# Kernel optimization log

Hardware: AMD Instinct MI355X
Metric: run time of the kernel (lower is better)

## Reference

```python
import jax, jax.numpy as jnp
import numpy as np

FEATURE = 1024
HIDDEN = 1024
BS = 64
T = 512


def setup_inputs() -> dict:
    key = jax.random.key(0)
    ks = jax.random.split(key, 5)
    # xavier_normal with gain=0.1: std = 0.1*sqrt(2/(fan_in+fan_out))
    std = 0.1 * np.sqrt(2.0 / (HIDDEN + FEATURE + HIDDEN))
    return {
        "x": jax.random.normal(ks[0], (BS, T, FEATURE), dtype=jnp.float32),
        "h_0": jax.random.normal(ks[1], (BS, HIDDEN), dtype=jnp.float32),
        "w_z": std * jax.random.normal(ks[2], (HIDDEN + FEATURE, HIDDEN), dtype=jnp.float32),
        "w_r": std * jax.random.normal(ks[3], (HIDDEN + FEATURE, HIDDEN), dtype=jnp.float32),
        "w": std * jax.random.normal(ks[4], (HIDDEN + FEATURE, HIDDEN), dtype=jnp.float32),
        "biasZ": jnp.zeros((HIDDEN,), dtype=jnp.float32),
        "biasR": jnp.zeros((HIDDEN,), dtype=jnp.float32),
        "biasHbar": jnp.zeros((HIDDEN,), dtype=jnp.float32),
    }


def reference(x, h_0, w_z, w_r, w, biasZ, biasR, biasHbar):
    # Split weights into h-part and x-part so the x contributions for z/r can be
    # precomputed for ALL timesteps in one big GEMM (same math as concat+matmul).
    H = h_0.shape[1]
    wz_h, wz_x = w_z[:H], w_z[H:]
    wr_h, wr_x = w_r[:H], w_r[H:]
    w_h, w_x = w[:H], w[H:]

    # (bs, T, hidden) precomputed x-side gate pre-activations
    xz = jnp.einsum('btf,fh->bth', x, wz_x) + biasZ
    xr = jnp.einsum('btf,fh->bth', x, wr_x) + biasR
    xh = jnp.einsum('btf,fh->bth', x, w_x) + biasHbar

    def step(h, inp):
        xz_t, xr_t, xh_t = inp
        z_t = jax.nn.sigmoid(h @ wz_h + xz_t)
        r_t = jax.nn.sigmoid(h @ wr_h + xr_t)
        hbar_t = jnp.tanh((r_t * h) @ w_h + xh_t)
        h_new = (1.0 - z_t) * h + z_t * hbar_t
        return h_new, h_new

    # scan over time (leading axis), inputs transposed to (T, bs, hidden)
    xs = (xz.swapaxes(0, 1), xr.swapaxes(0, 1), xh.swapaxes(0, 1))
    h_n, out_t = jax.lax.scan(step, h_0, xs)
    output = out_t.swapaxes(0, 1)  # (bs, T, hidden)
    return output, h_n
```

## Files before the change

### kernel.cpp

```cpp
#include <hip/hip_runtime.h>
#include <hip/hip_bf16.h>
#include <stdint.h>

#define BS 64
#define TT 512
#define FEAT 1024
#define HID 1024

__device__ __forceinline__ float sigmoidf_(float x){ return 1.0f/(1.0f + __expf(-x)); }

__device__ __forceinline__ unsigned short f2bf(float f){
    __hip_bfloat16 h = __float2bfloat16(f);
    return *reinterpret_cast<unsigned short*>(&h);
}
__device__ __forceinline__ float bf2f(unsigned short u){
    __hip_bfloat16 h = *reinterpret_cast<__hip_bfloat16*>(&u);
    return __bfloat162float(h);
}

__global__ __launch_bounds__(256) void p1_gemm(
    const float* __restrict__ x,
    const float* __restrict__ w_z, const float* __restrict__ w_r, const float* __restrict__ w,
    const float* __restrict__ bZ, const float* __restrict__ bR, const float* __restrict__ bH,
    float* __restrict__ xz32, float* __restrict__ xr32,
    unsigned short* __restrict__ xz16, unsigned short* __restrict__ xr16,
    float* __restrict__ xh, int use_bf)
{
    __shared__ float As[32][136];
    __shared__ float Bs[32][72];

    const int m0   = blockIdx.x * 128;
    const int n0g  = blockIdx.y * 64;
    const int mat  = n0g >> 10;
    const int ncol = n0g & 1023;

    const float* Wm    = (mat==0) ? w_z : (mat==1) ? w_r : w;
    const float* Bbase = Wm + (size_t)HID*1024 + ncol;
    const float* bias  = ((mat==0) ? bZ : (mat==1) ? bR : bH) + ncol;

    const int tid = threadIdx.x;
    const int tx = tid & 15, ty = tid >> 4;
    const int lm = tid >> 3;
    const int lk = (tid & 7) * 4;

    float acc[8][4];
    #pragma unroll
    for (int i=0;i<8;i++)
        #pragma unroll
        for (int j=0;j<4;j++) acc[i][j] = 0.f;

    for (int k0 = 0; k0 < 1024; k0 += 32) {
        #pragma unroll
        for (int h = 0; h < 4; ++h) {
            const int m = lm + 32*h;
            float4 a = *(const float4*)(x + (size_t)(m0+m)*1024 + k0 + lk);
            const float av[4] = {a.x, a.y, a.z, a.w};
            #pragma unroll
            for (int i=0;i<4;i++) {
                const int kk  = lk + i;
                const int col = m ^ (((kk>>2)&3) << 3);
                As[kk][col] = av[i];
            }
        }
        {
            const int kk = tid >> 3;
            const int nq = (tid & 7) * 4;
            float4 b0 = *(const float4*)(Bbase + (size_t)(k0+kk)*1024 + nq);
            float4 b1 = *(const float4*)(Bbase + (size_t)(k0+kk)*1024 + nq + 32);
            *(float4*)&Bs[kk][nq]      = b0;
            *(float4*)&Bs[kk][nq + 32] = b1;
        }
        __syncthreads();
        #pragma unroll
        for (int kk = 0; kk < 32; ++kk) {
            const int ablk = (ty ^ ((kk>>2)&3)) << 3;
            float4 a0 = *(const float4*)&As[kk][ablk];
            float4 a1 = *(const float4*)&As[kk][ablk + 4];
            float4 b4 = *(const float4*)&Bs[kk][tx*4];
            const float av[8] = {a0.x,a0.y,a0.z,a0.w,a1.x,a1.y,a1.z,a1.w};
            const float bv[4] = {b4.x,b4.y,b4.z,b4.w};
            #pragma unroll
            for (int i=0;i<8;i++)
                #pragma unroll
                for (int j=0;j<4;j++)
                    acc[i][j] = fmaf(av[i], bv[j], acc[i][j]);
        }
        __syncthreads();
    }

    float4 bb = *(const float4*)(bias + tx*4);
    const float badd[4] = {bb.x, bb.y, bb.z, bb.w};
    #pragma unroll
    for (int i=0;i<8;i++) {
        const int m = m0 + ty*8 + i;
        const size_t off = (size_t)m*1024 + ncol + tx*4;
        float v[4];
        #pragma unroll
        for (int j=0;j<4;j++) v[j] = acc[i][j] + badd[j];
        if (mat == 2) {
            float4 o; o.x=v[0]; o.y=v[1]; o.z=v[2]; o.w=v[3];
            *(float4*)(xh + off) = o;
        } else if (!use_bf) {
            float* dst = (mat==0) ? xz32 : xr32;
            float4 o; o.x=v[0]; o.y=v[1]; o.z=v[2]; o.w=v[3];
            *(float4*)(dst + off) = o;
        } else {
            unsigned short* dst = (mat==0) ? xz16 : xr16;
            ushort4 u; u.x=f2bf(v[0]); u.y=f2bf(v[1]); u.z=f2bf(v[2]); u.w=f2bf(v[3]);
            *(ushort4*)(dst + off) = u;
        }
    }
}

__global__ __launch_bounds__(256) void tr_h0(const float* __restrict__ h0, float* __restrict__ hT)
{
    const int g = blockIdx.x*256 + threadIdx.x;
    const int b = g >> 10, j = g & 1023;
    hT[j*64 + b] = h0[g];
}

__global__ __launch_bounds__(256) void k_gates(
    const float* __restrict__ hT,
    const float* __restrict__ w_z, const float* __restrict__ w_r,
    const float* __restrict__ xz32, const float* __restrict__ xr32,
    const unsigned short* __restrict__ xz16, const unsigned short* __restrict__ xr16,
    float* __restrict__ zT, float* __restrict__ rhT, int t, int use_bf)
{
    __shared__ float part[4][8][64];
    const int wg   = blockIdx.x;
    const int lane = threadIdx.x & 63;
    const int wv   = __builtin_amdgcn_readfirstlane(threadIdx.x >> 6);
    const bool isR = (wg >= 128);
    const float* W = isR ? w_r : w_z;
    const int ccol = (wg & 127) * 8;

    const float* wp = W  + (size_t)(wv*256)*1024 + ccol;
    const float* hp = hT + (size_t)(wv*256)*64   + lane;

    float acc[8] = {0,0,0,0,0,0,0,0};
    #pragma unroll 8
    for (int k = 0; k < 256; ++k) {
        const float hk = hp[(size_t)k*64];
        float4 wa = *(const float4*)(wp + (size_t)k*1024);
        float4 wb = *(const float4*)(wp + (size_t)k*1024 + 4);
        acc[0] = fmaf(hk, wa.x, acc[0]); acc[1] = fmaf(hk, wa.y, acc[1]);
        acc[2] = fmaf(hk, wa.z, acc[2]); acc[3] = fmaf(hk, wa.w, acc[3]);
        acc[4] = fmaf(hk, wb.x, acc[4]); acc[5] = fmaf(hk, wb.y, acc[5]);
        acc[6] = fmaf(hk, wb.z, acc[6]); acc[7] = fmaf(hk, wb.w, acc[7]);
    }
    #pragma unroll
    for (int c=0;c<8;c++) part[wv][c][lane] = acc[c];
    __syncthreads();

    #pragma unroll
    for (int e=0;e<2;e++) {
        const int o = threadIdx.x + e*256;
        const int c = o >> 6, b = o & 63;
        const float s = part[0][c][b] + part[1][c][b] + part[2][c][b] + part[3][c][b];
        const int j = ccol + c;
        const size_t xoff = ((size_t)b*TT + t)*1024 + j;
        if (!isR) {
            const float xv = use_bf ? bf2f(xz16[xoff]) : xz32[xoff];
            zT[j*64 + b] = sigmoidf_(s + xv);
        } else {
            const float xv = use_bf ? bf2f(xr16[xoff]) : xr32[xoff];
            rhT[j*64 + b] = sigmoidf_(s + xv) * hT[j*64 + b];
        }
    }
}

__global__ __launch_bounds__(256) void k_hbar(
    float* __restrict__ hT, const float* __restrict__ rhT, const float* __restrict__ zT,
    const float* __restrict__ w, float* __restrict__ out, int t, int is_last)
{
    __shared__ float part[4][4][64];
    const int wg   = blockIdx.x;
    const int lane = threadIdx.x & 63;
    const int wv   = __builtin_amdgcn_readfirstlane(threadIdx.x >> 6);
    const int c0   = wg * 4;

    const float* wp = w   + (size_t)(wv*256)*1024 + c0;
    const float* rp = rhT + (size_t)(wv*256)*64   + lane;

    float acc[4] = {0,0,0,0};
    #pragma unroll 8
    for (int k = 0; k < 256; ++k) {
        const float rk = rp[(size_t)k*64];
        float4 wa = *(const float4*)(wp + (size_t)k*1024);
        acc[0] = fmaf(rk, wa.x, acc[0]); acc[1] = fmaf(rk, wa.y, acc[1]);
        acc[2] = fmaf(rk, wa.z, acc[2]); acc[3] = fmaf(rk, wa.w, acc[3]);
    }
    #pragma unroll
    for (int c=0;c<4;c++) part[wv][c][lane] = acc[c];
    __syncthreads();

    const int o = threadIdx.x;
    const int c = o >> 6, b = o & 63;
    const float s = part[0][c][b] + part[1][c][b] + part[2][c][b] + part[3][c][b];
    const int j = c0 + c;
    const size_t ooff = ((size_t)b*TT + t)*1024 + j;
    const float hb   = tanhf(s + out[ooff]);
    const float z    = zT[j*64 + b];
    const float hold = hT[j*64 + b];
    const float hn   = (1.f - z)*hold + z*hb;
    hT[j*64 + b] = hn;
    out[ooff]    = hn;
    if (is_last) out[(size_t)BS*TT*1024 + (size_t)b*1024 + j] = hn;
}

extern "C" void kernel_launch(void* const* d_in, const int* in_sizes, int n_in,
                              void* d_out, int out_size, void* d_ws, size_t ws_size,
                              hipStream_t stream)
{
    const float* x   = (const float*)d_in[0];
    const float* h0  = (const float*)d_in[1];
    const float* w_z = (const float*)d_in[2];
    const float* w_r = (const float*)d_in[3];
    const float* w   = (const float*)d_in[4];
    const float* bZ  = (const float*)d_in[5];
    const float* bR  = (const float*)d_in[6];
    const float* bH  = (const float*)d_in[7];
    float* out = (float*)d_out;

    const size_t nBT = (size_t)BS*TT*1024;
    const size_t need32 = (2*nBT + 3*65536) * 4;
    const int use_bf = (ws_size < need32) ? 1 : 0;

    char* wsb = (char*)d_ws;
    float *xz32 = nullptr, *xr32 = nullptr;
    unsigned short *xz16 = nullptr, *xr16 = nullptr;
    float *hT, *zT, *rhT;
    if (!use_bf) {
        xz32 = (float*)wsb;
        xr32 = xz32 + nBT;
        hT   = xr32 + nBT;
    } else {
        xz16 = (unsigned short*)wsb;
        xr16 = xz16 + nBT;
        hT   = (float*)(wsb + 2*nBT*sizeof(unsigned short));
    }
    zT  = hT + 65536;
    rhT = zT + 65536;

    p1_gemm<<<dim3(256,48), 256, 0, stream>>>(x, w_z, w_r, w, bZ, bR, bH,
                                              xz32, xr32, xz16, xr16, out, use_bf);
    tr_h0<<<256, 256, 0, stream>>>(h0, hT);
    for (int t = 0; t < TT; ++t) {
        k_gates<<<256, 256, 0, stream>>>(hT, w_z, w_r, xz32, xr32, xz16, xr16, zT, rhT, t, use_bf);
        k_hbar <<<256, 256, 0, stream>>>(hT, rhT, zT, w, out, t, (t == TT-1) ? 1 : 0);
    }
}
```

Measured before the change: 26.87 ms.

## Replace per-timestep kernel launches with persistent cooperative scan kernel

```diff
diff --git a/kernel.cpp b/kernel.cpp
--- a/kernel.cpp
+++ b/kernel.cpp
@@ -1,11 +1,16 @@
 #include <hip/hip_runtime.h>
 #include <hip/hip_bf16.h>
+#include <hip/hip_cooperative_groups.h>
 #include <stdint.h>
 
 #define BS 64
 #define TT 512
 #define FEAT 1024
 #define HID 1024
+#define NWG 256
+#define NTHR 512
+
+namespace cg = cooperative_groups;
 
 __device__ __forceinline__ float sigmoidf_(float x){ return 1.0f/(1.0f + __expf(-x)); }
 
@@ -22,9 +27,8 @@
     const float* __restrict__ x,
     const float* __restrict__ w_z, const float* __restrict__ w_r, const float* __restrict__ w,
     const float* __restrict__ bZ, const float* __restrict__ bR, const float* __restrict__ bH,
-    float* __restrict__ xz32, float* __restrict__ xr32,
     unsigned short* __restrict__ xz16, unsigned short* __restrict__ xr16,
-    float* __restrict__ xh, int use_bf)
+    float* __restrict__ xh)
 {
     __shared__ float As[32][136];
     __shared__ float Bs[32][72];
@@ -100,10 +104,6 @@
         if (mat == 2) {
             float4 o; o.x=v[0]; o.y=v[1]; o.z=v[2]; o.w=v[3];
             *(float4*)(xh + off) = o;
-        } else if (!use_bf) {
-            float* dst = (mat==0) ? xz32 : xr32;
-            float4 o; o.x=v[0]; o.y=v[1]; o.z=v[2]; o.w=v[3];
-            *(float4*)(dst + off) = o;
         } else {
             unsigned short* dst = (mat==0) ? xz16 : xr16;
             ushort4 u; u.x=f2bf(v[0]); u.y=f2bf(v[1]); u.z=f2bf(v[2]); u.w=f2bf(v[3]);
@@ -112,100 +112,114 @@
     }
 }
 
-__global__ __launch_bounds__(256) void tr_h0(const float* __restrict__ h0, float* __restrict__ hT)
+__global__ __launch_bounds__(NTHR, 1) void scan_persist(
+    const float* __restrict__ h0,
+    const float* __restrict__ w_z, const float* __restrict__ w_r, const float* __restrict__ w,
+    const unsigned short* __restrict__ xz16, const unsigned short* __restrict__ xr16,
+    float* __restrict__ hT, float* __restrict__ rhT, float* __restrict__ out)
 {
-    const int g = blockIdx.x*256 + threadIdx.x;
-    const int b = g >> 10, j = g & 1023;
-    hT[j*64 + b] = h0[g];
-}
-
-__global__ __launch_bounds__(256) void k_gates(
-    const float* __restrict__ hT,
-    const float* __restrict__ w_z, const float* __restrict__ w_r,
-    const float* __restrict__ xz32, const float* __restrict__ xr32,
-    const unsigned short* __restrict__ xz16, const unsigned short* __restrict__ xr16,
-    float* __restrict__ zT, float* __restrict__ rhT, int t, int use_bf)
-{
-    __shared__ float part[4][8][64];
-    const int wg   = blockIdx.x;
-    const int lane = threadIdx.x & 63;
-    const int wv   = __builtin_amdgcn_readfirstlane(threadIdx.x >> 6);
-    const bool isR = (wg >= 128);
-    const float* W = isR ? w_r : w_z;
-    const int ccol = (wg & 127) * 8;
-
-    const float* wp = W  + (size_t)(wv*256)*1024 + ccol;
-    const float* hp = hT + (size_t)(wv*256)*64   + lane;
-
-    float acc[8] = {0,0,0,0,0,0,0,0};
-    #pragma unroll 8
-    for (int k = 0; k < 256; ++k) {
-        const float hk = hp[(size_t)k*64];
-        float4 wa = *(const float4*)(wp + (size_t)k*1024);
-        float4 wb = *(const float4*)(wp + (size_t)k*1024 + 4);
-        acc[0] = fmaf(hk, wa.x, acc[0]); acc[1] = fmaf(hk, wa.y, acc[1]);
-        acc[2] = fmaf(hk, wa.z, acc[2]); acc[3] = fmaf(hk, wa.w, acc[3]);
-        acc[4] = fmaf(hk, wb.x, acc[4]); acc[5] = fmaf(hk, wb.y, acc[5]);
-        acc[6] = fmaf(hk, wb.z, acc[6]); acc[7] = fmaf(hk, wb.w, acc[7]);
-    }
-    #pragma unroll
-    for (int c=0;c<8;c++) part[wv][c][lane] = acc[c];
-    __syncthreads();
-
-    #pragma unroll
-    for (int e=0;e<2;e++) {
-        const int o = threadIdx.x + e*256;
-        const int c = o >> 6, b = o & 63;
-        const float s = part[0][c][b] + part[1][c][b] + part[2][c][b] + part[3][c][b];
-        const int j = ccol + c;
-        const size_t xoff = ((size_t)b*TT + t)*1024 + j;
-        if (!isR) {
-            const float xv = use_bf ? bf2f(xz16[xoff]) : xz32[xoff];
-            zT[j*64 + b] = sigmoidf_(s + xv);
-        } else {
-            const float xv = use_bf ? bf2f(xr16[xoff]) : xr32[xoff];
-            rhT[j*64 + b] = sigmoidf_(s + xv) * hT[j*64 + b];
-        }
-    }
-}
-
-__global__ __launch_bounds__(256) void k_hbar(
-    float* __restrict__ hT, const float* __restrict__ rhT, const float* __restrict__ zT,
-    const float* __restrict__ w, float* __restrict__ out, int t, int is_last)
-{
-    __shared__ float part[4][4][64];
-    const int wg   = blockIdx.x;
-    const int lane = threadIdx.x & 63;
-    const int wv   = __builtin_amdgcn_readfirstlane(threadIdx.x >> 6);
-    const int c0   = wg * 4;
-
-    const float* wp = w   + (size_t)(wv*256)*1024 + c0;
-    const float* rp = rhT + (size_t)(wv*256)*64   + lane;
-
-    float acc[4] = {0,0,0,0};
-    #pragma unroll 8
-    for (int k = 0; k < 256; ++k) {
-        const float rk = rp[(size_t)k*64];
-        float4 wa = *(const float4*)(wp + (size_t)k*1024);
-        acc[0] = fmaf(rk, wa.x, acc[0]); acc[1] = fmaf(rk, wa.y, acc[1]);
-        acc[2] = fmaf(rk, wa.z, acc[2]); acc[3] = fmaf(rk, wa.w, acc[3]);
-    }
-    #pragma unroll
-    for (int c=0;c<4;c++) part[wv][c][lane] = acc[c];
-    __syncthreads();
-
-    const int o = threadIdx.x;
-    const int c = o >> 6, b = o & 63;
-    const float s = part[0][c][b] + part[1][c][b] + part[2][c][b] + part[3][c][b];
-    const int j = c0 + c;
-    const size_t ooff = ((size_t)b*TT + t)*1024 + j;
-    const float hb   = tanhf(s + out[ooff]);
-    const float z    = zT[j*64 + b];
-    const float hold = hT[j*64 + b];
-    const float hn   = (1.f - z)*hold + z*hb;
-    hT[j*64 + b] = hn;
-    out[ooff]    = hn;
-    if (is_last) out[(size_t)BS*TT*1024 + (size_t)b*1024 + j] = hn;
+    cg::grid_group grid = cg::this_grid();
+
+    __shared__ float lwz[1024*4];
+    __shared__ float lwr[1024*4];
+    __shared__ float lwh[1024*4];
+    __shared__ float part[8*8*64];
+    __shared__ float zs[4*64];
+
+    const int wg  = blockIdx.x;
+    const int tid = threadIdx.x;
+    const int c0  = wg * 4;
+    const int q   = tid >> 6;
+    const int b   = tid & 63;
+
+    for (int k = tid; k < 1024; k += NTHR) {
+        *(float4*)&lwz[k*4] = *(const float4*)(w_z + (size_t)k*1024 + c0);
+        *(float4*)&lwr[k*4] = *(const float4*)(w_r + (size_t)k*1024 + c0);
+        *(float4*)&lwh[k*4] = *(const float4*)(w   + (size_t)k*1024 + c0);
+    }
+    {
+        const int g0 = wg * NTHR + tid;
+        if (g0 < HID*BS) {
+            const int bb = g0 >> 10, jj = g0 & 1023;
+            hT[jj*64 + bb] = h0[g0];
+        }
+    }
+    grid.sync();
+
+    for (int t = 0; t < TT; ++t) {
+        {
+            float az0=0.f,az1=0.f,az2=0.f,az3=0.f;
+            float ar0=0.f,ar1=0.f,ar2=0.f,ar3=0.f;
+            const float*  hp  = hT + (size_t)(q*128)*64 + b;
+            const float4* wzp = (const float4*)&lwz[(q*128)*4];
+            const float4* wrp = (const float4*)&lwr[(q*128)*4];
+            #pragma unroll 8
+            for (int kk = 0; kk < 128; ++kk) {
+                const float hk = hp[(size_t)kk*64];
+                const float4 wz4 = wzp[kk];
+                const float4 wr4 = wrp[kk];
+                az0 = fmaf(hk, wz4.x, az0); az1 = fmaf(hk, wz4.y, az1);
+                az2 = fmaf(hk, wz4.z, az2); az3 = fmaf(hk, wz4.w, az3);
+                ar0 = fmaf(hk, wr4.x, ar0); ar1 = fmaf(hk, wr4.y, ar1);
+                ar2 = fmaf(hk, wr4.z, ar2); ar3 = fmaf(hk, wr4.w, ar3);
+            }
+            part[(q*8+0)*64+b] = az0; part[(q*8+1)*64+b] = az1;
+            part[(q*8+2)*64+b] = az2; part[(q*8+3)*64+b] = az3;
+            part[(q*8+4)*64+b] = ar0; part[(q*8+5)*64+b] = ar1;
+            part[(q*8+6)*64+b] = ar2; part[(q*8+7)*64+b] = ar3;
+        }
+        __syncthreads();
+        {
+            const int a  = tid >> 6;
+            const int bb = tid & 63;
+            float s = 0.f;
+            #pragma unroll
+            for (int qq = 0; qq < 8; ++qq) s += part[(qq*8+a)*64+bb];
+            if (a < 4) {
+                const size_t xoff = ((size_t)bb*TT + t)*1024 + c0 + a;
+                zs[a*64+bb] = sigmoidf_(s + bf2f(xz16[xoff]));
+            } else {
+                const int c = a - 4;
+                const size_t xoff = ((size_t)bb*TT + t)*1024 + c0 + c;
+                const float rv = sigmoidf_(s + bf2f(xr16[xoff]));
+                rhT[(c0+c)*64 + bb] = rv * hT[(c0+c)*64 + bb];
+            }
+        }
+        grid.sync();
+
+        {
+            float ah0=0.f,ah1=0.f,ah2=0.f,ah3=0.f;
+            const float*  rp  = rhT + (size_t)(q*128)*64 + b;
+            const float4* whp = (const float4*)&lwh[(q*128)*4];
+            #pragma unroll 8
+            for (int kk = 0; kk < 128; ++kk) {
+                const float rk = rp[(size_t)kk*64];
+                const float4 w4 = whp[kk];
+                ah0 = fmaf(rk, w4.x, ah0); ah1 = fmaf(rk, w4.y, ah1);
+                ah2 = fmaf(rk, w4.z, ah2); ah3 = fmaf(rk, w4.w, ah3);
+            }
+            part[(q*4+0)*64+b] = ah0; part[(q*4+1)*64+b] = ah1;
+            part[(q*4+2)*64+b] = ah2; part[(q*4+3)*64+b] = ah3;
+        }
+        __syncthreads();
+        if (tid < 256) {
+            const int c  = tid >> 6;
+            const int bb = tid & 63;
+            float s = 0.f;
+            #pragma unroll
+            for (int qq = 0; qq < 8; ++qq) s += part[(qq*4+c)*64+bb];
+            const size_t ooff = ((size_t)bb*TT + t)*1024 + c0 + c;
+            const float hbar = tanhf(s + out[ooff]);
+            const float zv   = zs[c*64+bb];
+            const int   hoff = (c0+c)*64 + bb;
+            const float hold = hT[hoff];
+            const float hn   = fmaf(zv, hbar - hold, hold);
+            hT[hoff]  = hn;
+            out[ooff] = hn;
+            if (t == TT-1) out[(size_t)BS*TT*1024 + (size_t)bb*1024 + c0 + c] = hn;
+        }
+        grid.sync();
+    }
 }
 
 extern "C" void kernel_launch(void* const* d_in, const int* in_sizes, int n_in,
@@ -223,30 +237,20 @@
     float* out = (float*)d_out;
 
     const size_t nBT = (size_t)BS*TT*1024;
-    const size_t need32 = (2*nBT + 3*65536) * 4;
-    const int use_bf = (ws_size < need32) ? 1 : 0;
-
     char* wsb = (char*)d_ws;
-    float *xz32 = nullptr, *xr32 = nullptr;
-    unsigned short *xz16 = nullptr, *xr16 = nullptr;
-    float *hT, *zT, *rhT;
-    if (!use_bf) {
-        xz32 = (float*)wsb;
-        xr32 = xz32 + nBT;
-        hT   = xr32 + nBT;
-    } else {
-        xz16 = (unsigned short*)wsb;
-        xr16 = xz16 + nBT;
-        hT   = (float*)(wsb + 2*nBT*sizeof(unsigned short));
-    }
-    zT  = hT + 65536;
-    rhT = zT + 65536;
+    unsigned short* xz16 = (unsigned short*)wsb;
+    unsigned short* xr16 = xz16 + nBT;
+    float* hT  = (float*)(wsb + 2*nBT*sizeof(unsigned short));
+    float* rhT = hT + HID*BS;
 
     p1_gemm<<<dim3(256,48), 256, 0, stream>>>(x, w_z, w_r, w, bZ, bR, bH,
-                                              xz32, xr32, xz16, xr16, out, use_bf);
-    tr_h0<<<256, 256, 0, stream>>>(h0, hT);
-    for (int t = 0; t < TT; ++t) {
-        k_gates<<<256, 256, 0, stream>>>(hT, w_z, w_r, xz32, xr32, xz16, xr16, zT, rhT, t, use_bf);
-        k_hbar <<<256, 256, 0, stream>>>(hT, rhT, zT, w, out, t, (t == TT-1) ? 1 : 0);
-    }
-}
+                                              xz16, xr16, out);
+
+    const float* h0a = h0; const float* wza = w_z; const float* wra = w_r;
+    const float* wa = w; const unsigned short* xza = xz16; const unsigned short* xra = xr16;
+    float* hTa = hT; float* rhTa = rhT; float* outa = out;
+    void* args[] = { (void*)&h0a, (void*)&wza, (void*)&wra, (void*)&wa,
+                     (void*)&xza, (void*)&xra, (void*)&hTa, (void*)&rhTa, (void*)&outa };
+    hipLaunchCooperativeKernel((void*)scan_persist, dim3(NWG), dim3(NTHR),
+                               args, 0, stream);
+}
```

Result: slower. 41.07 ms (+52.9%).
